# Performance work log

Measured on AMD Instinct MI355X. Metric: run time of the kernel, lower is better.

The kernel has to match this reference:

```python
import jax, jax.numpy as jnp
import numpy as np
import math

SR = 96000.0
FRAME = 2048          # FRAME_SIZE
NB = 16               # N_BIQUADS
B, F = 16, 128        # batch, n_frames
N = F * FRAME         # n_samples (divisible by FRAME)

GAIN_RANGE = (-24.0, 24.0)
BROADBAND = (-60.0, 0.0)
Q_RANGE = (0.5, 16.0)
HPF_R = (20.0, 500.0)
LPF_R = (5000.0, 20000.0)
SHELF_R = (50.0, 16000.0)
PEAK_R = (100.0, 15000.0)


def _denorm_freq(n, r):
    lo, hi = math.log(r[0]), math.log(r[1])
    return jnp.exp(lo + n * (hi - lo))


def _denorm_gain(n, r):
    return r[0] + n * (r[1] - r[0])


def _denorm_q(n):
    lo, hi = math.log(Q_RANGE[0]), math.log(Q_RANGE[1])
    return jnp.exp(lo + n * (hi - lo))


def _norm(b0, b1, b2, a0, a1, a2):
    return b0 / a0, b1 / a0, b2 / a0, a1 / a0, a2 / a0


def _hp(fc, Q):
    w0 = 2 * math.pi * fc / SR
    al = jnp.sin(w0) / (2 * Q)
    c = jnp.cos(w0)
    return _norm((1 + c) / 2, -(1 + c), (1 + c) / 2, 1 + al, -2 * c, 1 - al)


def _lp(fc, Q):
    w0 = 2 * math.pi * fc / SR
    al = jnp.sin(w0) / (2 * Q)
    c = jnp.cos(w0)
    return _norm((1 - c) / 2, 1 - c, (1 - c) / 2, 1 + al, -2 * c, 1 - al)


def _peak(fc, g_db, Q):
    A = jnp.power(10.0, g_db / 40.0)
    w0 = 2 * math.pi * fc / SR
    al = jnp.sin(w0) / (2 * Q)
    c = jnp.cos(w0)
    return _norm(1 + al * A, -2 * c, 1 - al * A, 1 + al / A, -2 * c, 1 - al / A)


def _lowshelf(fc, g_db, Q):
    A = jnp.power(10.0, g_db / 40.0)
    w0 = 2 * math.pi * fc / SR
    al = jnp.sin(w0) / (2 * Q)
    c = jnp.cos(w0)
    sA = jnp.sqrt(A)
    b0 = A * (A + 1 - (A - 1) * c + 2 * sA * al)
    b1 = 2 * A * (A - 1 - (A + 1) * c)
    b2 = A * (A + 1 - (A - 1) * c - 2 * sA * al)
    a0 = A + 1 + (A - 1) * c + 2 * sA * al
    a1 = -2 * (A - 1 + (A + 1) * c)
    a2 = A + 1 + (A - 1) * c - 2 * sA * al
    return _norm(b0, b1, b2, a0, a1, a2)


def _highshelf(fc, g_db, Q):
    A = jnp.power(10.0, g_db / 40.0)
    w0 = 2 * math.pi * fc / SR
    al = jnp.sin(w0) / (2 * Q)
    c = jnp.cos(w0)
    sA = jnp.sqrt(A)
    b0 = A * (A + 1 + (A - 1) * c + 2 * sA * al)
    b1 = -2 * A * (A - 1 + (A + 1) * c)
    b2 = A * (A + 1 + (A - 1) * c - 2 * sA * al)
    a0 = A + 1 - (A - 1) * c + 2 * sA * al
    a1 = 2 * (A - 1 - (A + 1) * c)
    a2 = A + 1 - (A - 1) * c - 2 * sA * al
    return _norm(b0, b1, b2, a0, a1, a2)


def _forward(audio, params):
    b, n = audio.shape
    f = n // FRAME
    fp = params.shape[2]
    # per-audio-frame parameter index: min(frame_idx, n_frames_params-1)
    idx = jnp.minimum(jnp.arange(f), fp - 1)
    p = params[:, :, idx]                       # (B, 50, F)
    bq = p[:, : NB * 3, :].reshape(b, NB, 3, f)  # (B, 16, 3, F)
    in_g = jnp.power(10.0, _denorm_gain(p[:, -2, :], BROADBAND) / 20.0)   # (B,F)
    out_g = jnp.power(10.0, _denorm_gain(p[:, -1, :], BROADBAND) / 20.0)  # (B,F)

    x = audio.reshape(b, f, FRAME) * in_g[:, :, None]

    # per-stage normalized coefficients, each (B, F)
    coefs = []
    for i in range(NB):
        fn, gn, qn = bq[:, i, 0], bq[:, i, 1], bq[:, i, 2]
        Q = _denorm_q(qn)
        if i == 0:                      # BIQUAD_HPF
            c = _hp(_denorm_freq(fn, HPF_R), Q)
        elif i == NB - 1:               # BIQUAD_LPF
            c = _lp(_denorm_freq(fn, LPF_R), Q)
        elif i == 1:                    # BIQUAD_LOW_SHELF
            c = _lowshelf(_denorm_freq(fn, SHELF_R), _denorm_gain(gn, GAIN_RANGE), Q)
        elif i == NB - 2:               # BIQUAD_HIGH_SHELF
            c = _highshelf(_denorm_freq(fn, SHELF_R), _denorm_gain(gn, GAIN_RANGE), Q)
        else:                           # peaking EQ
            c = _peak(_denorm_freq(fn, PEAK_R), _denorm_gain(gn, GAIN_RANGE), Q)
        coefs.append(jnp.stack(c))      # (5, B, F)
    C = jnp.stack(coefs).reshape(NB, 5, b * f)  # (16, 5, B*F)

    # each (batch, frame) lane filters independently with zero initial state
    xt = x.reshape(b * f, FRAME).T              # (T, B*F)

    def step(s, v):
        # s: (16, 2, B*F) DF2T states; v: (B*F,) cascade input
        new_s = []
        for i in range(NB):
            b0, b1, b2, a1, a2 = C[i, 0], C[i, 1], C[i, 2], C[i, 3], C[i, 4]
            y = b0 * v + s[i, 0]
            s1 = b1 * v - a1 * y + s[i, 1]
            s2 = b2 * v - a2 * y
            new_s.append(jnp.stack([s1, s2]))
            v = y
        return jnp.stack(new_s), v

    s0 = jnp.zeros((NB, 2, b * f), dtype=audio.dtype)
    _, ys = jax.lax.scan(step, s0, xt)          # (T, B*F)

    y = ys.T.reshape(b, f, FRAME) * out_g[:, :, None]
    return y.reshape(b, n)


def setup_inputs() -> dict:
    key = jax.random.key(0)
    k1, k2 = jax.random.split(key)
    audio = jax.random.normal(k1, (B, N), dtype=jnp.float32)
    params = jax.random.uniform(k2, (B, 50, F), dtype=jnp.float32)
    return {"audio": audio, "params": params}


def reference(audio, params):
    return _forward(audio, params)
```

## Files before the change

### kernel.cpp

```cpp
#include <hip/hip_runtime.h>
#include <math.h>

namespace {

constexpr int kNB    = 16;
constexpr int kFrame = 2048;
constexpr int kHalf  = 16;

typedef float f32x2 __attribute__((ext_vector_type(2)));

__device__ inline f32x2 pk_fma(f32x2 a, f32x2 b, f32x2 c) {
    f32x2 d;
    asm("v_pk_fma_f32 %0, %1, %2, %3" : "=v"(d) : "v"(a), "v"(b), "v"(c));
    return d;
}
__device__ inline f32x2 pk_mul(f32x2 a, f32x2 b) {
    f32x2 d;
    asm("v_pk_mul_f32 %0, %1, %2" : "=v"(d) : "v"(a), "v"(b));
    return d;
}
__device__ inline f32x2 pk_add(f32x2 a, f32x2 b) {
    f32x2 d;
    asm("v_pk_add_f32 %0, %1, %2" : "=v"(d) : "v"(a), "v"(b));
    return d;
}

template <int CTRL>
__device__ inline float dpp_f(float v) {
    return __int_as_float(
        __builtin_amdgcn_update_dpp(0, __float_as_int(v), CTRL, 0xF, 0xF, true));
}

template <int CTRL>
__device__ inline void ks_level(float& v0, float& v1, const float4 M, const float na1) {
    const float t0 = dpp_f<CTRL>(v0);
    const float t1 = dpp_f<CTRL>(v1);
    const float w  = fmaf(na1, t0, t1);
    v0 = fmaf(M.x, w,  fmaf(M.y, t0, v0));
    v1 = fmaf(M.z, t0, fmaf(M.y, t1, v1));
}

__global__ __launch_bounds__(64)
void biquad_chain_kernel(const float* __restrict__ audio,
                         const float* __restrict__ params,
                         float* __restrict__ out)
{
    __shared__ float4 sK[kNB][2];
    __shared__ float4 powT[kNB][33];

    const int lane = threadIdx.x & 63;
    const int ch   = blockIdx.x;
    const int bb   = ch >> 7;
    const int ff   = ch & 127;

    const float* pb = params + (size_t)bb * (50 * 128) + ff;

    {
        const int band = lane & 15;
        const int part = lane >> 4;
        const double fn = (double)pb[(band * 3 + 0) * 128];
        const double gn = (double)pb[(band * 3 + 1) * 128];
        const double qn = (double)pb[(band * 3 + 2) * 128];
        const double PI   = 3.14159265358979323846;
        const double LN10 = 2.302585092994046;

        const bool isHP = (band == 0), isLP = (band == kNB - 1);
        const bool isShelf = (band == 1) || (band == kNB - 2);
        const double flo = isHP ? 2.995732273553991
                        : isLP ? 8.517193191416238
                        : isShelf ? 3.912023005428146
                        : 4.605170185988092;
        const double fsp = isHP ? 3.2188758248682006
                        : isLP ? 1.3862943611198906
                        : isShelf ? 5.768320995793772
                        : 5.0106352940962555;

        const double Q  = exp(-0.6931471805599453 + qn * 3.4657359027997265);
        const double fc = exp(flo + fn * fsp);
        const double w0 = (2.0 * PI / 96000.0) * fc;
        const double sw = sin(w0);
        const double cw = cos(w0);
        const double al = sw / (2.0 * Q);
        const double gdb = (isHP || isLP) ? 0.0 : (-24.0 + gn * 48.0);
        const double A   = exp(gdb * (LN10 / 40.0));
        const double sA  = sqrt(A);
        const double ge = isHP ? (-60.0 + (double)pb[48 * 128] * 60.0) * (LN10 / 20.0)
                        : isLP ? (-60.0 + (double)pb[49 * 128] * 60.0) * (LN10 / 20.0)
                        : 0.0;
        const double gm = exp(ge);

        double b0, b1, b2, a0, a1, a2;
        if (isHP) {
            b0 = (1.0 + cw) * 0.5; b1 = -(1.0 + cw); b2 = (1.0 + cw) * 0.5;
            a0 = 1.0 + al; a1 = -2.0 * cw; a2 = 1.0 - al;
        } else if (isLP) {
            b0 = (1.0 - cw) * 0.5; b1 = 1.0 - cw; b2 = (1.0 - cw) * 0.5;
            a0 = 1.0 + al; a1 = -2.0 * cw; a2 = 1.0 - al;
        } else if (band == 1) {
            const double s2 = 2.0 * sA * al;
            b0 = A * ((A + 1.0) - (A - 1.0) * cw + s2);
            b1 = 2.0 * A * ((A - 1.0) - (A + 1.0) * cw);
            b2 = A * ((A + 1.0) - (A - 1.0) * cw - s2);
            a0 = (A + 1.0) + (A - 1.0) * cw + s2;
            a1 = -2.0 * ((A - 1.0) + (A + 1.0) * cw);
            a2 = (A + 1.0) + (A - 1.0) * cw - s2;
        } else if (band == kNB - 2) {
            const double s2 = 2.0 * sA * al;
            b0 = A * ((A + 1.0) + (A - 1.0) * cw + s2);
            b1 = -2.0 * A * ((A - 1.0) + (A + 1.0) * cw);
            b2 = A * ((A + 1.0) + (A - 1.0) * cw - s2);
            a0 = (A + 1.0) - (A - 1.0) * cw + s2;
            a1 = 2.0 * ((A - 1.0) - (A + 1.0) * cw);
            a2 = (A + 1.0) - (A - 1.0) * cw - s2;
        } else {
            b0 = 1.0 + al * A; b1 = -2.0 * cw; b2 = 1.0 - al * A;
            a0 = 1.0 + al / A; a1 = -2.0 * cw; a2 = 1.0 - al / A;
        }
        const double inv  = 1.0 / a0;
        const double binv = inv * gm;
        b0 *= binv; b1 *= binv; b2 *= binv; a1 *= inv; a2 *= inv;

        double alc = 1.0, bec = 0.0;
        double al16 = 0, be16 = 0, al32 = 0, be32 = 0;
        double al256 = 0, be256 = 0, al512 = 0, be512 = 0;
        #pragma unroll
        for (int k = 1; k <= 9; ++k) {
            const double a_ = alc, b_ = bec;
            alc = a_ * (2.0 * b_ - a1 * a_);
            bec = b_ * b_ - a2 * (a_ * a_);
            if (k == 4) { al16 = alc; be16 = bec; }
            if (k == 5) { al32 = alc; be32 = bec; }
            if (k == 8) { al256 = alc; be256 = bec; }
            if (k == 9) { al512 = alc; be512 = bec; }
        }
        auto cmp = [&](double alx, double bex, double aly, double bey,
                       double& alo, double& beo) {
            const double p = alx * aly;
            alo = alx * bey + bex * aly - a1 * p;
            beo = bex * bey - a2 * p;
        };

        double Sa, Sb;
        if (part == 0)      { Sa = al32; Sb = be32; }
        else if (part == 1) { cmp(al256, be256, al32, be32, Sa, Sb); }
        else if (part == 2) { cmp(al512, be512, al32, be32, Sa, Sb); }
        else { double ta, tb; cmp(al512, be512, al256, be256, ta, tb);
               cmp(ta, tb, al32, be32, Sa, Sb); }

        #pragma unroll
        for (int j = 0; j < 8; ++j) {
            powT[band][8 * part + j] =
                float4{(float)Sa, (float)Sb, (float)(-a2 * Sa), 0.f};
            double na, nb;
            cmp(Sa, Sb, al32, be32, na, nb);
            Sa = na; Sb = nb;
        }
        if (part == 0) {
            sK[band][0] = float4{(float)b0, (float)b1, (float)b2, (float)(-a1)};
            sK[band][1] = float4{(float)(-a2), (float)al16, (float)be16,
                                 (float)(-a2 * al16)};
        }
    }
    __syncthreads();

    f32x2 X[kHalf];
    {
        const float4* ap = reinterpret_cast<const float4*>(
            audio + (size_t)ch * kFrame + lane * 32);
        #pragma unroll
        for (int k = 0; k < 4; ++k) {
            const float4 va = ap[k];
            const float4 vb = ap[k + 4];
            X[4 * k + 0] = f32x2{va.x, vb.x};
            X[4 * k + 1] = f32x2{va.y, vb.y};
            X[4 * k + 2] = f32x2{va.z, vb.z};
            X[4 * k + 3] = f32x2{va.w, vb.w};
        }
    }

    for (int band = 0; band < kNB; ++band) {
        const float4 k0 = sK[band][0];
        const float4 k1 = sK[band][1];
        const float4 P1 = powT[band][0];
        const float4 P2 = powT[band][1];
        const float4 P4 = powT[band][3];
        const float4 P8 = powT[band][7];
        const float4 Pme = powT[band][lane & 15];
        const float4 Qme = powT[band][lane & 31];

        const float b0 = k0.x, b1 = k0.y, b2 = k0.z, na1 = k0.w;
        const float na2 = k1.x, al16 = k1.y, be16 = k1.z, ga16 = k1.w;
        const f32x2 b0p  = {b0, b0},  b1p = {b1, b1}, b2p = {b2, b2};
        const f32x2 na1p = {na1, na1}, na2p = {na2, na2};

        f32x2 s1 = {0.f, 0.f}, s2 = {0.f, 0.f};
        #pragma unroll
        for (int t = 0; t < kHalf; ++t) {
            const f32x2 xv = X[t];
            const f32x2 y  = pk_fma(b0p, xv, s1);
            const f32x2 tm = pk_fma(b1p, xv, s2);
            s2 = pk_fma(na2p, y, pk_mul(b2p, xv));
            s1 = pk_fma(na1p, y, tm);
            X[t] = y;
        }

        const float wf = fmaf(na1, s1.x, s2.x);
        const float d0 = fmaf(al16, wf, fmaf(be16, s1.x, s1.y));
        const float d1 = fmaf(ga16, s1.x, fmaf(be16, s2.x, s2.y));

        float v0 = dpp_f<0x138>(d0);
        float v1 = dpp_f<0x138>(d1);
        ks_level<0x111>(v0, v1, P1, na1);
        ks_level<0x112>(v0, v1, P2, na1);
        ks_level<0x114>(v0, v1, P4, na1);
        ks_level<0x118>(v0, v1, P8, na1);
        {
            float t0 = dpp_f<0x142>(v0);
            float t1 = dpp_f<0x142>(v1);
            const bool g = (lane & 16) != 0;
            t0 = g ? t0 : 0.f;
            t1 = g ? t1 : 0.f;
            const float w = fmaf(na1, t0, t1);
            v0 = fmaf(Pme.x, w,  fmaf(Pme.y, t0, v0));
            v1 = fmaf(Pme.z, t0, fmaf(Pme.y, t1, v1));
        }
        {
            float t0 = dpp_f<0x143>(v0);
            float t1 = dpp_f<0x143>(v1);
            const bool g = lane >= 32;
            t0 = g ? t0 : 0.f;
            t1 = g ? t1 : 0.f;
            const float w = fmaf(na1, t0, t1);
            v0 = fmaf(Qme.x, w,  fmaf(Qme.y, t0, v0));
            v1 = fmaf(Qme.z, t0, fmaf(Qme.y, t1, v1));
        }

        const float wr  = fmaf(na1, v0, v1);
        const float uB0 = fmaf(al16, wr, fmaf(be16, v0, s1.x));
        const float uB1 = fmaf(ga16, v0, fmaf(be16, v1, s2.x));

        f32x2 w0 = {v0, uB0}, w1 = {v1, uB1};
        #pragma unroll
        for (int t = 0; t < kHalf; ++t) {
            const f32x2 c = w0;
            X[t] = pk_add(X[t], c);
            w0 = pk_fma(na1p, c, w1);
            w1 = pk_mul(na2p, c);
        }
    }

    {
        float4* op = reinterpret_cast<float4*>(out + (size_t)ch * kFrame + lane * 32);
        #pragma unroll
        for (int k = 0; k < 4; ++k) {
            op[k]     = float4{X[4 * k + 0].x, X[4 * k + 1].x, X[4 * k + 2].x, X[4 * k + 3].x};
            op[k + 4] = float4{X[4 * k + 0].y, X[4 * k + 1].y, X[4 * k + 2].y, X[4 * k + 3].y};
        }
    }
}

}

extern "C" void kernel_launch(void* const* d_in, const int* in_sizes, int n_in,
                              void* d_out, int out_size, void* d_ws, size_t ws_size,
                              hipStream_t stream)
{
    (void)d_ws; (void)ws_size; (void)n_in; (void)in_sizes;
    const float* audio  = (const float*)d_in[0];
    const float* params = (const float*)d_in[1];
    float* outp = (float*)d_out;

    const int channels = out_size / kFrame;
    hipLaunchKernelGGL(biquad_chain_kernel, dim3(channels), dim3(64), 0, stream,
                       audio, params, outp);
}
```

Baseline: 26.45 us.

## Fuse band correction pass with next band's local filter; compute coefficients in float

Moves biquad coefficient setup from double precision to float, replacing sin/cos with a polynomial half-angle sine and fast exp, which cuts expensive FP64 transcendental work in the prologue. It also merges each band's carry-correction loop with the next band's zero-state local filtering loop, so the 16-sample block is traversed once per band instead of twice. This gives more interleaved independent work and fewer register reads and writes of X. The cost is lower coefficient accuracy and a more complex loop structure.

```diff
diff --git a/kernel.cpp b/kernel.cpp
--- a/kernel.cpp
+++ b/kernel.cpp
@@ -58,76 +58,86 @@
     {
         const int band = lane & 15;
         const int part = lane >> 4;
-        const double fn = (double)pb[(band * 3 + 0) * 128];
-        const double gn = (double)pb[(band * 3 + 1) * 128];
-        const double qn = (double)pb[(band * 3 + 2) * 128];
-        const double PI   = 3.14159265358979323846;
-        const double LN10 = 2.302585092994046;
+        const float fn = pb[(band * 3 + 0) * 128];
+        const float gn = pb[(band * 3 + 1) * 128];
+        const float qn = pb[(band * 3 + 2) * 128];
 
         const bool isHP = (band == 0), isLP = (band == kNB - 1);
         const bool isShelf = (band == 1) || (band == kNB - 2);
-        const double flo = isHP ? 2.995732273553991
-                        : isLP ? 8.517193191416238
-                        : isShelf ? 3.912023005428146
-                        : 4.605170185988092;
-        const double fsp = isHP ? 3.2188758248682006
-                        : isLP ? 1.3862943611198906
-                        : isShelf ? 5.768320995793772
-                        : 5.0106352940962555;
-
-        const double Q  = exp(-0.6931471805599453 + qn * 3.4657359027997265);
-        const double fc = exp(flo + fn * fsp);
-        const double w0 = (2.0 * PI / 96000.0) * fc;
-        const double sw = sin(w0);
-        const double cw = cos(w0);
-        const double al = sw / (2.0 * Q);
-        const double gdb = (isHP || isLP) ? 0.0 : (-24.0 + gn * 48.0);
-        const double A   = exp(gdb * (LN10 / 40.0));
-        const double sA  = sqrt(A);
-        const double ge = isHP ? (-60.0 + (double)pb[48 * 128] * 60.0) * (LN10 / 20.0)
-                        : isLP ? (-60.0 + (double)pb[49 * 128] * 60.0) * (LN10 / 20.0)
-                        : 0.0;
-        const double gm = exp(ge);
-
-        double b0, b1, b2, a0, a1, a2;
+        const float flo = isHP ? 2.995732274f
+                        : isLP ? 8.517193191f
+                        : isShelf ? 3.912023005f
+                        : 4.605170186f;
+        const float fsp = isHP ? 3.218875825f
+                        : isLP ? 1.386294361f
+                        : isShelf ? 5.768320996f
+                        : 5.010635294f;
+
+        const float Q  = __expf(fmaf(qn, 3.465735903f, -0.6931471806f));
+        const float fc = __expf(fmaf(fn, fsp, flo));
+        const float hw = fc * 3.272492349e-5f;
+        const float x2 = hw * hw;
+        const float sh = hw * fmaf(x2, fmaf(x2, fmaf(x2, -1.984126984e-4f,
+                                   8.333333333e-3f), -0.1666666667f), 1.0f);
+        const float chh = sqrtf(fmaf(-sh, sh, 1.0f));
+        const float sw  = 2.0f * sh * chh;
+        const float ver = 2.0f * sh * sh;
+        const float alq = sw / (Q + Q);
+        const float gdb = (isHP || isLP) ? 0.f : fmaf(gn, 48.f, -24.f);
+        const float A   = __expf(gdb * 0.05756462732f);
+        const float sA  = sqrtf(A);
+        const float ge  = isHP ? fmaf(pb[48 * 128], 60.f, -60.f) * 0.1151292546f
+                        : isLP ? fmaf(pb[49 * 128], 60.f, -60.f) * 0.1151292546f
+                        : 0.f;
+        const float gm  = __expf(ge);
+
+        float b0, b1, b2, a0, a1, a2;
         if (isHP) {
-            b0 = (1.0 + cw) * 0.5; b1 = -(1.0 + cw); b2 = (1.0 + cw) * 0.5;
-            a0 = 1.0 + al; a1 = -2.0 * cw; a2 = 1.0 - al;
+            b0 = 1.0f - 0.5f * ver; b1 = ver - 2.0f; b2 = b0;
+            a0 = 1.0f + alq; a1 = 2.0f * ver - 2.0f; a2 = 1.0f - alq;
         } else if (isLP) {
-            b0 = (1.0 - cw) * 0.5; b1 = 1.0 - cw; b2 = (1.0 - cw) * 0.5;
-            a0 = 1.0 + al; a1 = -2.0 * cw; a2 = 1.0 - al;
+            b0 = 0.5f * ver; b1 = ver; b2 = b0;
+            a0 = 1.0f + alq; a1 = 2.0f * ver - 2.0f; a2 = 1.0f - alq;
         } else if (band == 1) {
-            const double s2 = 2.0 * sA * al;
-            b0 = A * ((A + 1.0) - (A - 1.0) * cw + s2);
-            b1 = 2.0 * A * ((A - 1.0) - (A + 1.0) * cw);
-            b2 = A * ((A + 1.0) - (A - 1.0) * cw - s2);
-            a0 = (A + 1.0) + (A - 1.0) * cw + s2;
-            a1 = -2.0 * ((A - 1.0) + (A + 1.0) * cw);
-            a2 = (A + 1.0) + (A - 1.0) * cw - s2;
+            const float t = 2.0f * sA * alq;
+            const float u = (A - 1.0f) * ver;
+            const float w = (A + 1.0f) * ver;
+            b0 = A * (2.0f + u + t);
+            b1 = A * (2.0f * w - 4.0f);
+            b2 = A * (2.0f + u - t);
+            a0 = 2.0f * A - u + t;
+            a1 = 2.0f * w - 4.0f * A;
+            a2 = 2.0f * A - u - t;
         } else if (band == kNB - 2) {
-            const double s2 = 2.0 * sA * al;
-            b0 = A * ((A + 1.0) + (A - 1.0) * cw + s2);
-            b1 = -2.0 * A * ((A - 1.0) + (A + 1.0) * cw);
-            b2 = A * ((A + 1.0) + (A - 1.0) * cw - s2);
-            a0 = (A + 1.0) - (A - 1.0) * cw + s2;
-            a1 = 2.0 * ((A - 1.0) - (A + 1.0) * cw);
-            a2 = (A + 1.0) - (A - 1.0) * cw - s2;
+            const float t = 2.0f * sA * alq;
+            const float u = (A - 1.0f) * ver;
+            const float w = (A + 1.0f) * ver;
+            b0 = A * (2.0f * A - u + t);
+            b1 = -2.0f * A * (2.0f * A - w);
+            b2 = A * (2.0f * A - u - t);
+            a0 = 2.0f + u + t;
+            a1 = 2.0f * w - 4.0f;
+            a2 = 2.0f + u - t;
         } else {
-            b0 = 1.0 + al * A; b1 = -2.0 * cw; b2 = 1.0 - al * A;
-            a0 = 1.0 + al / A; a1 = -2.0 * cw; a2 = 1.0 - al / A;
-        }
-        const double inv  = 1.0 / a0;
-        const double binv = inv * gm;
-        b0 *= binv; b1 *= binv; b2 *= binv; a1 *= inv; a2 *= inv;
-
+            const float alA  = alq * A;
+            const float aloA = alq / A;
+            b0 = 1.0f + alA; b1 = 2.0f * ver - 2.0f; b2 = 1.0f - alA;
+            a0 = 1.0f + aloA; a1 = b1; a2 = 1.0f - aloA;
+        }
+        const float inv  = 1.0f / a0;
+        const float binv = inv * gm;
+        b0 *= binv; b1 *= binv; b2 *= binv;
+        a1 *= inv; a2 *= inv;
+
+        const double a1d = (double)a1, a2d = (double)a2;
         double alc = 1.0, bec = 0.0;
         double al16 = 0, be16 = 0, al32 = 0, be32 = 0;
         double al256 = 0, be256 = 0, al512 = 0, be512 = 0;
         #pragma unroll
         for (int k = 1; k <= 9; ++k) {
             const double a_ = alc, b_ = bec;
-            alc = a_ * (2.0 * b_ - a1 * a_);
-            bec = b_ * b_ - a2 * (a_ * a_);
+            alc = a_ * (2.0 * b_ - a1d * a_);
+            bec = b_ * b_ - a2d * (a_ * a_);
             if (k == 4) { al16 = alc; be16 = bec; }
             if (k == 5) { al32 = alc; be32 = bec; }
             if (k == 8) { al256 = alc; be256 = bec; }
@@ -136,8 +146,8 @@
         auto cmp = [&](double alx, double bex, double aly, double bey,
                        double& alo, double& beo) {
             const double p = alx * aly;
-            alo = alx * bey + bex * aly - a1 * p;
-            beo = bex * bey - a2 * p;
+            alo = alx * bey + bex * aly - a1d * p;
+            beo = bex * bey - a2d * p;
         };
 
         double Sa, Sb;
@@ -150,15 +160,15 @@
         #pragma unroll
         for (int j = 0; j < 8; ++j) {
             powT[band][8 * part + j] =
-                float4{(float)Sa, (float)Sb, (float)(-a2 * Sa), 0.f};
+                float4{(float)Sa, (float)Sb, (float)(-a2d * Sa), 0.f};
             double na, nb;
             cmp(Sa, Sb, al32, be32, na, nb);
             Sa = na; Sb = nb;
         }
         if (part == 0) {
-            sK[band][0] = float4{(float)b0, (float)b1, (float)b2, (float)(-a1)};
-            sK[band][1] = float4{(float)(-a2), (float)al16, (float)be16,
-                                 (float)(-a2 * al16)};
+            sK[band][0] = float4{b0, b1, b2, -a1};
+            sK[band][1] = float4{-a2, (float)al16, (float)be16,
+                                 (float)(-a2d * al16)};
         }
     }
     __syncthreads();
@@ -178,31 +188,31 @@
         }
     }
 
+    float4 k0 = sK[0][0], k1 = sK[0][1];
+    f32x2 b0p  = {k0.x, k0.x}, b1p = {k0.y, k0.y}, b2p = {k0.z, k0.z};
+    f32x2 na1p = {k0.w, k0.w}, na2p = {k1.x, k1.x};
+
+    f32x2 s1 = {0.f, 0.f}, s2 = {0.f, 0.f};
+    #pragma unroll
+    for (int t = 0; t < kHalf; ++t) {
+        const f32x2 xv = X[t];
+        const f32x2 y  = pk_fma(b0p, xv, s1);
+        const f32x2 tm = pk_fma(b1p, xv, s2);
+        s2 = pk_fma(na2p, y, pk_mul(b2p, xv));
+        s1 = pk_fma(na1p, y, tm);
+        X[t] = y;
+    }
+
     for (int band = 0; band < kNB; ++band) {
-        const float4 k0 = sK[band][0];
-        const float4 k1 = sK[band][1];
+        const float na1 = na1p.x;
+        const float al16 = k1.y, be16 = k1.z, ga16 = k1.w;
+
         const float4 P1 = powT[band][0];
         const float4 P2 = powT[band][1];
         const float4 P4 = powT[band][3];
         const float4 P8 = powT[band][7];
         const float4 Pme = powT[band][lane & 15];
         const float4 Qme = powT[band][lane & 31];
-
-        const float b0 = k0.x, b1 = k0.y, b2 = k0.z, na1 = k0.w;
-        const float na2 = k1.x, al16 = k1.y, be16 = k1.z, ga16 = k1.w;
-        const f32x2 b0p  = {b0, b0},  b1p = {b1, b1}, b2p = {b2, b2};
-        const f32x2 na1p = {na1, na1}, na2p = {na2, na2};
-
-        f32x2 s1 = {0.f, 0.f}, s2 = {0.f, 0.f};
-        #pragma unroll
-        for (int t = 0; t < kHalf; ++t) {
-            const f32x2 xv = X[t];
-            const f32x2 y  = pk_fma(b0p, xv, s1);
-            const f32x2 tm = pk_fma(b1p, xv, s2);
-            s2 = pk_fma(na2p, y, pk_mul(b2p, xv));
-            s1 = pk_fma(na1p, y, tm);
-            X[t] = y;
-        }
 
         const float wf = fmaf(na1, s1.x, s2.x);
         const float d0 = fmaf(al16, wf, fmaf(be16, s1.x, s1.y));
@@ -238,15 +248,41 @@
         const float wr  = fmaf(na1, v0, v1);
         const float uB0 = fmaf(al16, wr, fmaf(be16, v0, s1.x));
         const float uB1 = fmaf(ga16, v0, fmaf(be16, v1, s2.x));
-
-        f32x2 w0 = {v0, uB0}, w1 = {v1, uB1};
+        f32x2 cw0 = {v0, uB0}, cw1 = {v1, uB1};
+
+        if (band == kNB - 1) {
+            #pragma unroll
+            for (int t = 0; t < kHalf; ++t) {
+                const f32x2 cc = cw0;
+                X[t] = pk_add(X[t], cc);
+                cw0 = pk_fma(na1p, cc, cw1);
+                cw1 = pk_mul(na2p, cc);
+            }
+            break;
+        }
+
+        const float4 nk0 = sK[band + 1][0];
+        const float4 nk1 = sK[band + 1][1];
+        const f32x2 nb0p  = {nk0.x, nk0.x}, nb1p = {nk0.y, nk0.y};
+        const f32x2 nb2p  = {nk0.z, nk0.z};
+        const f32x2 nna1p = {nk0.w, nk0.w}, nna2p = {nk1.x, nk1.x};
+
+        s1 = f32x2{0.f, 0.f}; s2 = f32x2{0.f, 0.f};
         #pragma unroll
         for (int t = 0; t < kHalf; ++t) {
-            const f32x2 c = w0;
-            X[t] = pk_add(X[t], c);
-            w0 = pk_fma(na1p, c, w1);
-            w1 = pk_mul(na2p, c);
-        }
+            const f32x2 cc = cw0;
+            cw0 = pk_fma(na1p, cc, cw1);
+            cw1 = pk_mul(na2p, cc);
+            const f32x2 xv = pk_add(X[t], cc);
+            const f32x2 y  = pk_fma(nb0p, xv, s1);
+            const f32x2 tm = pk_fma(nb1p, xv, s2);
+            s2 = pk_fma(nna2p, y, pk_mul(nb2p, xv));
+            s1 = pk_fma(nna1p, y, tm);
+            X[t] = y;
+        }
+
+        k0 = nk0; k1 = nk1;
+        b0p = nb0p; b1p = nb1p; b2p = nb2p; na1p = nna1p; na2p = nna2p;
     }
 
     {
```

Measured after the change: 28.00 us. 5.9% more time.
